# Kernel tuning notes

Measured on AMD Instinct MI355X. Metric: run time of the kernel, lower is better.

## Reference

```python
import jax, jax.numpy as jnp
import numpy as np

N = 131072      # total nodes
B = 16          # graphs in batch (num_segments)
C = 128         # in_channels
K = 16          # n_super_nodes
TAU = 1.0
PRUNING_THRESHOLD = 0.01
SPARSITY_WEIGHT = 0.01
TEMPORAL_W = 0.1 * 5
COLLAPSE_W = 2.0
EPS = 1e-9


def setup_inputs() -> dict:
    key = jax.random.key(0)
    ks = jax.random.split(key, 8)
    x = jax.random.normal(ks[0], (N, C), dtype=jnp.float32)
    batch = jnp.sort(jax.random.randint(ks[1], (N,), 0, B)).astype(jnp.int64)
    pos = jax.random.normal(ks[2], (N, 2), dtype=jnp.float32)
    # Gumbel noise for gumbel_softmax (sampled once, passed as input for determinism)
    gumbel = jax.random.gumbel(ks[3], (N, K), dtype=jnp.float32)
    # assign_mlp params: Linear(C,C) -> ReLU -> Linear(C,K)
    W1 = jax.random.normal(ks[4], (C, C), dtype=jnp.float32) / np.sqrt(C)
    b1 = jnp.zeros((C,), dtype=jnp.float32)
    W2 = jax.random.normal(ks[5], (K, C), dtype=jnp.float32) / np.sqrt(C)
    b2 = jnp.zeros((K,), dtype=jnp.float32)
    scaling = jnp.asarray(10.0, dtype=jnp.float32)
    active_mask = jnp.ones((K,), dtype=jnp.float32)  # buffer, starts all-active
    return {"x": x, "batch": batch, "pos": pos, "gumbel": gumbel,
            "W1": W1, "b1": b1, "W2": W2, "b2": b2,
            "scaling": scaling, "active_mask": active_mask}


def reference(x, batch, pos, gumbel, W1, b1, W2, b2, scaling, active_mask):
    # --- assignment logits: MLP * scaling (eval mode, prev_assignments=None) ---
    h = jax.nn.relu(x @ W1.T + b1)            # [N, C]
    logits = (h @ W2.T + b2) * scaling        # [N, K]
    # eval-path masking: masked_fill(mask == 0, -1e9)
    masked_logits = jnp.where(active_mask[None, :] == 0.0, -1e9, logits)
    # gumbel_softmax (soft, hard=False)
    s = jax.nn.softmax((masked_logits + gumbel) / TAU, axis=-1)   # [N, K]

    avg_s = jnp.mean(s, axis=0)               # [K]

    # --- losses ---
    entropy = -jnp.mean(jnp.sum(s * jnp.log(s + EPS), axis=1))
    uniform_p = 1.0 / K
    diversity = jnp.sum(uniform_p * jnp.log(uniform_p / (avg_s + EPS)))
    pruning = jnp.mean(jnp.abs(avg_s * (1.0 - active_mask)))
    sparsity = (jnp.sum(active_mask) / K) * SPARSITY_WEIGHT
    temporal = jnp.asarray(0.0, jnp.float32)  # prev_assignments is None
    # collapse-prevention / balance bodies are truncated upstream; faithful proxies
    collapse = jnp.sum((avg_s - uniform_p) ** 2) * COLLAPSE_W
    balance = jnp.std(avg_s)
    spatial = jnp.asarray(0.0, jnp.float32)

    # --- pooled features: out[b,k,c] = sum_{n in graph b} s[n,k] * x[n,c] ---
    weighted = x[:, None, :] * s[:, :, None]                  # [N, K, C]
    out = jax.ops.segment_sum(weighted, batch, num_segments=B)  # [B, K, C]

    # --- super-node positions ---
    w_pos = pos[:, None, :] * s[:, :, None]                    # [N, K, 2]
    sum_s_pos = jax.ops.segment_sum(w_pos, batch, num_segments=B)  # [B, K, 2]
    sum_s = jax.ops.segment_sum(s, batch, num_segments=B)[..., None] + EPS  # [B, K, 1]
    mu = sum_s_pos / sum_s                                     # [B, K, 2]

    # --- separation loss: pairwise repulsion between super-node centers ---
    dist_sq = jnp.sum((mu[:, :, None, :] - mu[:, None, :, :]) ** 2, axis=-1)  # [B,K,K]
    eye = jnp.eye(K, dtype=mu.dtype)[None]
    repulsion = 1.0 / (dist_sq + 1.0)
    separation = jnp.sum(repulsion * (1.0 - eye)) / (K * (K - 1))

    losses = jnp.stack([entropy, diversity, spatial, pruning, sparsity,
                        temporal * TEMPORAL_W, collapse, balance, separation])
    return out, s, mu, losses
```

## Files before the change

kernel.cpp:

```cpp
#include <hip/hip_runtime.h>
#include <hip/hip_bf16.h>
#include <math.h>

#define NN 131072
#define BSEG 16
#define CCH 128
#define KK 16
#define EPSF 1e-9f
#define XST 136

#define OFF_S   32768
#define OFF_MU  2129920
#define OFF_L   2130432

#define REDC_BASE 1024
#define REDC_STRIDE 1024
#define NRED 64
#define ST_BASE (REDC_BASE + NRED * REDC_STRIDE)
#define NST 8
#define ST_SZ (BSEG * KK * CCH)

#define TILES 2

typedef __bf16 bf16x8 __attribute__((ext_vector_type(8)));
typedef float  f32x4  __attribute__((ext_vector_type(4)));
typedef float  f32x16 __attribute__((ext_vector_type(16)));

__device__ __forceinline__ int load_batch(const void* bptr, int n, int is64) {
    if (is64) return (int)((const long long*)bptr)[n];
    return ((const int*)bptr)[n];
}

__device__ __forceinline__ float wave_sum(float v) {
#pragma unroll
    for (int o = 32; o > 0; o >>= 1) v += __shfl_xor(v, o, 64);
    return v;
}

__device__ __forceinline__ bf16x8 pack8(float4 a, float4 b) {
    bf16x8 v;
    v[0] = (__bf16)a.x; v[1] = (__bf16)a.y; v[2] = (__bf16)a.z; v[3] = (__bf16)a.w;
    v[4] = (__bf16)b.x; v[5] = (__bf16)b.y; v[6] = (__bf16)b.z; v[7] = (__bf16)b.w;
    return v;
}

__global__ void k_zero(float* __restrict__ ws, const int* __restrict__ b32) {
    int i = blockIdx.x * 256 + threadIdx.x;
    ws[REDC_BASE + i] = 0.0f;
    if (i == 0) ws[0] = (b32[NN - 1] == 0) ? 1.0f : 0.0f;
}

__global__ __launch_bounds__(256, 2) void k_fused(
    const float* __restrict__ x, const void* __restrict__ batch,
    const float* __restrict__ pos, const float* __restrict__ gumbel,
    const float* __restrict__ W1, const float* __restrict__ b1,
    const float* __restrict__ W2, const float* __restrict__ b2,
    const float* __restrict__ scaling, const float* __restrict__ active_mask,
    float* __restrict__ s_out, float* __restrict__ ws)
{
    __shared__ __align__(16) __bf16 x_lds[128 * XST];
    __shared__ __align__(16) __bf16 h_lds[128 * XST];
    __shared__ __align__(16) __bf16 sT[16 * XST];
    __shared__ float2 pos_lds[128];
    __shared__ int bsegs[128];

    const int tid  = threadIdx.x;
    const int lane = tid & 63;
    const int wv   = tid >> 6;
    const int is64 = (int)ws[0];

    float* rc  = ws + REDC_BASE + (size_t)(blockIdx.x & (NRED - 1)) * REDC_STRIDE;
    float* stg = ws + ST_BASE   + (size_t)(blockIdx.x & (NST  - 1)) * ST_SZ;

    bf16x8 bfr[8];
    {
        const float* wrow = W1 + (size_t)(wv * 32 + (lane & 31)) * CCH + (lane >> 5) * 8;
#pragma unroll
        for (int ks = 0; ks < 8; ks++) {
            float4 u = *(const float4*)(wrow + ks * 16);
            float4 v = *(const float4*)(wrow + ks * 16 + 4);
            bfr[ks] = pack8(u, v);
        }
    }
    const float b1j = b1[wv * 32 + (lane & 31)];

    f32x4 pacc[2];
#pragma unroll
    for (int t = 0; t < 2; t++)
#pragma unroll
        for (int r = 0; r < 4; r++) pacc[t][r] = 0.0f;
    int curseg = -1;

    for (int t = 0; t < TILES; t++) {
        const int n0 = blockIdx.x * (TILES * 128) + t * 128;

        if (t) __syncthreads();

        if (tid < 128) {
            bsegs[tid] = load_batch(batch, n0 + tid, is64);
            pos_lds[tid] = ((const float2*)pos)[n0 + tid];
        }
        const int nd = lane & 15;
        const int g  = lane >> 4;
        float4 gu[2];
        {
#pragma unroll
            for (int tt = 0; tt < 2; tt++) {
                int node = (wv * 2 + tt) * 16 + nd;
                gu[tt] = *(const float4*)(gumbel + (size_t)(n0 + node) * KK + g * 4);
            }
        }
        {
            const float4* xg = (const float4*)(x + (size_t)n0 * CCH);
#pragma unroll
            for (int i = 0; i < 8; i++) {
                int p = i * 256 + tid;
                float4 a = xg[2 * p], b = xg[2 * p + 1];
                *(bf16x8*)&x_lds[(p >> 4) * XST + (p & 15) * 8] = pack8(a, b);
            }
        }
        __syncthreads();

        {
            f32x16 acc[4];
#pragma unroll
            for (int mt = 0; mt < 4; mt++)
#pragma unroll
                for (int r = 0; r < 16; r++) acc[mt][r] = 0.0f;

#pragma unroll
            for (int ks = 0; ks < 8; ks++) {
#pragma unroll
                for (int mt = 0; mt < 4; mt++) {
                    bf16x8 a = *(bf16x8*)&x_lds[(size_t)(mt * 32 + (lane & 31)) * XST + ks * 16 + (lane >> 5) * 8];
                    acc[mt] = __builtin_amdgcn_mfma_f32_32x32x16_bf16(a, bfr[ks], acc[mt], 0, 0, 0);
                }
            }
#pragma unroll
            for (int mt = 0; mt < 4; mt++)
#pragma unroll
                for (int r = 0; r < 16; r++) {
                    int node = mt * 32 + (r & 3) + 8 * (r >> 2) + 4 * (lane >> 5);
                    h_lds[(size_t)node * XST + wv * 32 + (lane & 31)] = (__bf16)fmaxf(acc[mt][r] + b1j, 0.0f);
                }
        }
        __syncthreads();

        {
            const int bf = bsegs[0], bl = bsegs[127];
            const float sc = scaling[0];
            float b2v[4], amv[4];
#pragma unroll
            for (int r = 0; r < 4; r++) { b2v[r] = b2[g * 4 + r]; amv[r] = active_mask[g * 4 + r]; }

            f32x4 acc2[2];
#pragma unroll
            for (int tt = 0; tt < 2; tt++)
#pragma unroll
                for (int r = 0; r < 4; r++) acc2[tt][r] = 0.0f;

#pragma unroll
            for (int ks = 0; ks < 4; ks++) {
                const float* w2row = W2 + (size_t)nd * CCH + ks * 32 + g * 8;
                float4 u = *(const float4*)w2row;
                float4 v4 = *(const float4*)(w2row + 4);
                bf16x8 bwf = pack8(u, v4);
#pragma unroll
                for (int tt = 0; tt < 2; tt++) {
                    bf16x8 a = *(bf16x8*)&h_lds[(size_t)((wv * 2 + tt) * 16 + nd) * XST + ks * 32 + g * 8];
                    acc2[tt] = __builtin_amdgcn_mfma_f32_16x16x32_bf16(bwf, a, acc2[tt], 0, 0, 0);
                }
            }

            float sA[4] = {0, 0, 0, 0}, pxA[4] = {0, 0, 0, 0}, pyA[4] = {0, 0, 0, 0};
            float sB[4] = {0, 0, 0, 0}, pxB[4] = {0, 0, 0, 0}, pyB[4] = {0, 0, 0, 0};
            float entacc = 0.0f;
            const bool dual = (bf != bl);

#pragma unroll
            for (int tt = 0; tt < 2; tt++) {
                const int node = (wv * 2 + tt) * 16 + nd;
                float v[4];
#pragma unroll
                for (int r = 0; r < 4; r++) {
                    float vv = (acc2[tt][r] + b2v[r]) * sc;
                    if (amv[r] == 0.0f) vv = -1e9f;
                    v[r] = vv + ((const float*)&gu[tt])[r];
                }
                float vm = fmaxf(fmaxf(v[0], v[1]), fmaxf(v[2], v[3]));
                vm = fmaxf(vm, __shfl_xor(vm, 16, 64));
                vm = fmaxf(vm, __shfl_xor(vm, 32, 64));
                float e[4];
                float ls = 0.0f;
#pragma unroll
                for (int r = 0; r < 4; r++) { e[r] = expf(v[r] - vm); ls += e[r]; }
                ls += __shfl_xor(ls, 16, 64);
                ls += __shfl_xor(ls, 32, 64);
                const float inv = 1.0f / ls;
                float s[4];
#pragma unroll
                for (int r = 0; r < 4; r++) s[r] = e[r] * inv;

                float4 so; so.x = s[0]; so.y = s[1]; so.z = s[2]; so.w = s[3];
                *(float4*)(s_out + (size_t)(n0 + node) * KK + g * 4) = so;
#pragma unroll
                for (int r = 0; r < 4; r++) sT[(g * 4 + r) * XST + node] = (__bf16)s[r];

#pragma unroll
                for (int r = 0; r < 4; r++) entacc += s[r] * logf(s[r] + EPSF);

                const float2 pp = pos_lds[node];
                const float w0 = (bsegs[node] == bf) ? 1.0f : 0.0f;
#pragma unroll
                for (int r = 0; r < 4; r++) {
                    const float sa = s[r] * w0;
                    sA[r] += sa; pxA[r] += sa * pp.x; pyA[r] += sa * pp.y;
                }
                if (dual) {
#pragma unroll
                    for (int r = 0; r < 4; r++) {
                        const float sb = s[r] * (1.0f - w0);
                        sB[r] += sb; pxB[r] += sb * pp.x; pyB[r] += sb * pp.y;
                    }
                }
            }

#pragma unroll
            for (int o = 1; o < 16; o <<= 1) {
#pragma unroll
                for (int r = 0; r < 4; r++) {
                    sA[r]  += __shfl_xor(sA[r],  o, 64);
                    pxA[r] += __shfl_xor(pxA[r], o, 64);
                    pyA[r] += __shfl_xor(pyA[r], o, 64);
                }
            }
            if (nd == 0) {
#pragma unroll
                for (int r = 0; r < 4; r++) {
                    const int k = g * 4 + r;
                    atomicAdd(&rc[bf * 16 + k], sA[r]);
                    atomicAdd(&rc[256 + bf * 32 + 2 * k],     pxA[r]);
                    atomicAdd(&rc[256 + bf * 32 + 2 * k + 1], pyA[r]);
                }
            }
            if (dual) {
#pragma unroll
                for (int o = 1; o < 16; o <<= 1) {
#pragma unroll
                    for (int r = 0; r < 4; r++) {
                        sB[r]  += __shfl_xor(sB[r],  o, 64);
                        pxB[r] += __shfl_xor(pxB[r], o, 64);
                        pyB[r] += __shfl_xor(pyB[r], o, 64);
                    }
                }
                if (nd == 0) {
#pragma unroll
                    for (int r = 0; r < 4; r++) {
                        const int k = g * 4 + r;
                        atomicAdd(&rc[bl * 16 + k], sB[r]);
                        atomicAdd(&rc[256 + bl * 32 + 2 * k],     pxB[r]);
                        atomicAdd(&rc[256 + bl * 32 + 2 * k + 1], pyB[r]);
                    }
                }
            }
            float entw = wave_sum(entacc);
            if (lane == 0) atomicAdd(&rc[768], entw);
        }
        __syncthreads();

        {
            const int bf = bsegs[0], bl = bsegs[127];
            const bool masked = (bf != bl);
            for (int seg = bf; seg <= bl; seg++) {
                if (seg != curseg) {
                    if (curseg >= 0) {
#pragma unroll
                        for (int tt = 0; tt < 2; tt++) {
#pragma unroll
                            for (int r = 0; r < 4; r++) {
                                int k = (lane >> 4) * 4 + r;
                                int c = (wv * 2 + tt) * 16 + (lane & 15);
                                atomicAdd(&stg[((size_t)curseg * KK + k) * CCH + c], pacc[tt][r]);
                            }
#pragma unroll
                            for (int r = 0; r < 4; r++) pacc[tt][r] = 0.0f;
                        }
                    }
                    curseg = seg;
                }
#pragma unroll
                for (int ks = 0; ks < 4; ks++) {
                    bf16x8 a = *(bf16x8*)&sT[(size_t)(lane & 15) * XST + ks * 32 + (lane >> 4) * 8];
                    if (masked) {
#pragma unroll
                        for (int i = 0; i < 8; i++) {
                            int ndd = ks * 32 + (lane >> 4) * 8 + i;
                            if (bsegs[ndd] != seg) a[i] = (__bf16)0.0f;
                        }
                    }
#pragma unroll
                    for (int tt = 0; tt < 2; tt++) {
                        int ct = wv * 2 + tt;
                        bf16x8 bx;
#pragma unroll
                        for (int i = 0; i < 8; i++)
                            bx[i] = x_lds[(size_t)(ks * 32 + (lane >> 4) * 8 + i) * XST + ct * 16 + (lane & 15)];
                        pacc[tt] = __builtin_amdgcn_mfma_f32_16x16x32_bf16(a, bx, pacc[tt], 0, 0, 0);
                    }
                }
            }
        }
    }

    if (curseg >= 0) {
#pragma unroll
        for (int tt = 0; tt < 2; tt++) {
#pragma unroll
            for (int r = 0; r < 4; r++) {
                int k = (lane >> 4) * 4 + r;
                int c = (wv * 2 + tt) * 16 + (lane & 15);
                atomicAdd(&stg[((size_t)curseg * KK + k) * CCH + c], pacc[tt][r]);
            }
        }
    }
}

__global__ __launch_bounds__(256) void k_tail(
    const float* __restrict__ ws, const float* __restrict__ active_mask,
    float* __restrict__ out, float* __restrict__ mu_out, float* __restrict__ losses)
{
    const int tid = threadIdx.x;

    if (blockIdx.x < 32) {
        int i = blockIdx.x * 256 + tid;
        float4 r = make_float4(0.f, 0.f, 0.f, 0.f);
#pragma unroll
        for (int c = 0; c < NST; c++) {
            float4 a = ((const float4*)(ws + ST_BASE + (size_t)c * ST_SZ))[i];
            r.x += a.x; r.y += a.y; r.z += a.z; r.w += a.w;
        }
        ((float4*)out)[i] = r;
        return;
    }

    __shared__ float lsum[256];
    __shared__ float lpos[512];
    __shared__ float lent[1];
    __shared__ float smu[512];
    __shared__ float savg[16];
    __shared__ float red[256];

    for (int a = tid; a < 769; a += 256) {
        float acc = 0.0f;
#pragma unroll 8
        for (int c = 0; c < NRED; c++) acc += ws[REDC_BASE + c * REDC_STRIDE + a];
        if (a < 256) lsum[a] = acc;
        else if (a < 768) lpos[a - 256] = acc;
        else lent[0] = acc;
    }
    __syncthreads();

    if (tid < 16) {
        float a = 0.0f;
#pragma unroll
        for (int b = 0; b < 16; b++) a += lsum[b * 16 + tid];
        savg[tid] = a / (float)NN;
    }
    for (int i = tid; i < 512; i += 256) {
        int sk = i >> 1;
        float v = lpos[i] / (lsum[sk] + EPSF);
        smu[i] = v;
        mu_out[i] = v;
    }
    __syncthreads();

    float rep = 0.0f;
    for (int t = tid; t < 4096; t += 256) {
        int b = t >> 8, i = (t >> 4) & 15, j = t & 15;
        if (i != j) {
            float dx = smu[b * 32 + i * 2]     - smu[b * 32 + j * 2];
            float dy = smu[b * 32 + i * 2 + 1] - smu[b * 32 + j * 2 + 1];
            rep += 1.0f / (dx * dx + dy * dy + 1.0f);
        }
    }
    red[tid] = rep;
    __syncthreads();
    for (int st = 128; st > 0; st >>= 1) {
        if (tid < st) red[tid] += red[tid + st];
        __syncthreads();
    }

    if (tid == 0) {
        const float p = 1.0f / 16.0f;
        float separation = red[0] / (float)(16 * 15);
        float entropy = -lent[0] / (float)NN;
        float diversity = 0.f, pruning = 0.f, amsum = 0.f, collapse = 0.f, mean = 0.f;
        for (int k = 0; k < 16; k++) {
            float a = savg[k];
            diversity += p * logf(p / (a + EPSF));
            pruning += fabsf(a * (1.0f - active_mask[k]));
            amsum += active_mask[k];
            collapse += (a - p) * (a - p);
            mean += a;
        }
        pruning /= 16.0f;
        mean /= 16.0f;
        float var = 0.f;
        for (int k = 0; k < 16; k++) { float d = savg[k] - mean; var += d * d; }
        float balance = sqrtf(var / 16.0f);
        float sparsity = (amsum / 16.0f) * 0.01f;
        collapse *= 2.0f;
        losses[0] = entropy;   losses[1] = diversity; losses[2] = 0.0f;
        losses[3] = pruning;   losses[4] = sparsity;  losses[5] = 0.0f;
        losses[6] = collapse;  losses[7] = balance;   losses[8] = separation;
    }
}

extern "C" void kernel_launch(void* const* d_in, const int* in_sizes, int n_in,
                              void* d_out, int out_size, void* d_ws, size_t ws_size,
                              hipStream_t stream) {
    const float* x       = (const float*)d_in[0];
    const void*  batch   = d_in[1];
    const float* pos     = (const float*)d_in[2];
    const float* gumbel  = (const float*)d_in[3];
    const float* W1      = (const float*)d_in[4];
    const float* b1      = (const float*)d_in[5];
    const float* W2      = (const float*)d_in[6];
    const float* b2      = (const float*)d_in[7];
    const float* scaling = (const float*)d_in[8];
    const float* am      = (const float*)d_in[9];

    float* out      = (float*)d_out;
    float* s_sec    = out + OFF_S;
    float* mu_sec   = out + OFF_MU;
    float* loss_sec = out + OFF_L;
    float* wsf      = (float*)d_ws;

    k_zero<<<1280, 256, 0, stream>>>(wsf, (const int*)batch);
    k_fused<<<NN / 256, 256, 0, stream>>>(x, batch, pos, gumbel, W1, b1, W2, b2,
                                          scaling, am, s_sec, wsf);
    k_tail<<<33, 256, 0, stream>>>(wsf, am, out, mu_sec, loss_sec);
}
```

Baseline: 156.7 us.

## Prefetch next tile's inputs into registers during pooling phase

For the second tile, the loads of x, gumbel, batch and pos are issued into registers right after the first tile's softmax stage, before that tile's pooling phase. They are then written into LDS at the start of the next iteration, so global-load latency overlaps with the pooling MFMA and atomic work. The cost is 16 extra float4 registers per thread plus extra gumbel and misc registers, which under launch_bounds(256,2) may cause spills or lower occupancy.

```diff
diff --git a/kernel.cpp b/kernel.cpp
--- a/kernel.cpp
+++ b/kernel.cpp
@@ -67,6 +67,8 @@
     const int tid  = threadIdx.x;
     const int lane = tid & 63;
     const int wv   = tid >> 6;
+    const int nd   = lane & 15;
+    const int g    = lane >> 4;
     const int is64 = (int)ws[0];
 
     float* rc  = ws + REDC_BASE + (size_t)(blockIdx.x & (NRED - 1)) * REDC_STRIDE;
@@ -91,32 +93,44 @@
         for (int r = 0; r < 4; r++) pacc[t][r] = 0.0f;
     int curseg = -1;
 
+    float4 xr[16];
+    float4 gup[2];
+    float4 guc[2];
+    int    bseg_r = 0;
+    float2 pos_r  = make_float2(0.f, 0.f);
+
+#pragma unroll
     for (int t = 0; t < TILES; t++) {
         const int n0 = blockIdx.x * (TILES * 128) + t * 128;
 
-        if (t) __syncthreads();
-
-        if (tid < 128) {
-            bsegs[tid] = load_batch(batch, n0 + tid, is64);
-            pos_lds[tid] = ((const float2*)pos)[n0 + tid];
-        }
-        const int nd = lane & 15;
-        const int g  = lane >> 4;
-        float4 gu[2];
-        {
+        if (t == 0) {
+            if (tid < 128) {
+                bsegs[tid] = load_batch(batch, n0 + tid, is64);
+                pos_lds[tid] = ((const float2*)pos)[n0 + tid];
+            }
 #pragma unroll
             for (int tt = 0; tt < 2; tt++) {
                 int node = (wv * 2 + tt) * 16 + nd;
-                gu[tt] = *(const float4*)(gumbel + (size_t)(n0 + node) * KK + g * 4);
-            }
-        }
-        {
+                guc[tt] = *(const float4*)(gumbel + (size_t)(n0 + node) * KK + g * 4);
+            }
             const float4* xg = (const float4*)(x + (size_t)n0 * CCH);
 #pragma unroll
             for (int i = 0; i < 8; i++) {
                 int p = i * 256 + tid;
                 float4 a = xg[2 * p], b = xg[2 * p + 1];
                 *(bf16x8*)&x_lds[(p >> 4) * XST + (p & 15) * 8] = pack8(a, b);
+            }
+        } else {
+            __syncthreads();
+            if (tid < 128) {
+                bsegs[tid] = bseg_r;
+                pos_lds[tid] = pos_r;
+            }
+            guc[0] = gup[0]; guc[1] = gup[1];
+#pragma unroll
+            for (int i = 0; i < 8; i++) {
+                int p = i * 256 + tid;
+                *(bf16x8*)&x_lds[(p >> 4) * XST + (p & 15) * 8] = pack8(xr[2 * i], xr[2 * i + 1]);
             }
         }
         __syncthreads();
@@ -185,7 +199,7 @@
                 for (int r = 0; r < 4; r++) {
                     float vv = (acc2[tt][r] + b2v[r]) * sc;
                     if (amv[r] == 0.0f) vv = -1e9f;
-                    v[r] = vv + ((const float*)&gu[tt])[r];
+                    v[r] = vv + ((const float*)&guc[tt])[r];
                 }
                 float vm = fmaxf(fmaxf(v[0], v[1]), fmaxf(v[2], v[3]));
                 vm = fmaxf(vm, __shfl_xor(vm, 16, 64));
@@ -267,6 +281,26 @@
             if (lane == 0) atomicAdd(&rc[768], entw);
         }
         __syncthreads();
+
+        if (t + 1 < TILES) {
+            const int n1 = n0 + 128;
+            if (tid < 128) {
+                bseg_r = load_batch(batch, n1 + tid, is64);
+                pos_r  = ((const float2*)pos)[n1 + tid];
+            }
+#pragma unroll
+            for (int tt = 0; tt < 2; tt++) {
+                int node = (wv * 2 + tt) * 16 + nd;
+                gup[tt] = *(const float4*)(gumbel + (size_t)(n1 + node) * KK + g * 4);
+            }
+            const float4* xg = (const float4*)(x + (size_t)n1 * CCH);
+#pragma unroll
+            for (int i = 0; i < 8; i++) {
+                int p = i * 256 + tid;
+                xr[2 * i]     = xg[2 * p];
+                xr[2 * i + 1] = xg[2 * p + 1];
+            }
+        }
 
         {
             const int bf = bsegs[0], bl = bsegs[127];
```

Measured after the change: 157.3 us. No clear change (+0.4%).
